# Kernel optimization log

Hardware: AMD Instinct MI355X
Metric: run time of the kernel (lower is better)

Reference implementation:

```python
import jax, jax.numpy as jnp
import numpy as np

B, T, D = 4, 2048, 1024
H = 16
DH = D // H

def setup_inputs() -> dict:
    key = jax.random.key(0)
    k1, k2, k3 = jax.random.split(key, 3)
    x = jax.random.normal(k1, (B, T, D), dtype=jnp.float32)
    causal_mask = jnp.tril(jnp.ones((T, T), dtype=bool))[None, None]  # (1,1,T,T)
    Wqkv = jax.random.normal(k2, (D, 3 * D), dtype=jnp.float32) * (1.0 / np.sqrt(D))
    Wout = jax.random.normal(k3, (D, D), dtype=jnp.float32) * (1.0 / np.sqrt(D))
    return {"x": x, "causal_mask": causal_mask, "Wqkv": Wqkv, "Wout": Wout}

def reference(x, causal_mask, Wqkv, Wout):
    Bb, Tt, C = x.shape
    scale = jnp.sqrt(jnp.asarray(DH, dtype=x.dtype))
    qkv = x @ Wqkv                                   # (B,T,3D)
    qkv = qkv.reshape(Bb, Tt, 3, H, DH)
    qkv = jnp.transpose(qkv, (2, 0, 3, 1, 4))        # (3,B,H,T,DH)
    q, k, v = qkv[0], qkv[1], qkv[2]
    attn = jnp.einsum('bhqd,bhkd->bhqk', q, k) / scale
    attn = jnp.where(causal_mask, attn, jnp.asarray(-jnp.inf, dtype=attn.dtype))
    attn = jax.nn.softmax(attn, axis=-1)             # dropout p=0 -> identity
    out = jnp.einsum('bhqk,bhkd->bhqd', attn, v)     # (B,H,T,DH)
    out = jnp.transpose(out, (0, 2, 1, 3)).reshape(Bb, Tt, C)
    return out @ Wout
```

## Files before the change

kernel.cpp:

```cpp
#include <hip/hip_runtime.h>
#include <hip/hip_bf16.h>
#include <math.h>


#define Bb 4
#define Tt 2048
#define Dd 1024
#define Hh 16
#define DH 64
#define Mrows (Bb*Tt)
#define NEGBIG (-1.0e30f)
#define KB64 (Dd/64)
#define CHUNKS 1024
#define TILEU16 8192

typedef unsigned short u16;
typedef __attribute__((ext_vector_type(8))) short bf16x8;
typedef __attribute__((ext_vector_type(4))) float f32x4;
typedef __attribute__((ext_vector_type(4))) unsigned int u32x4;

__device__ __forceinline__ u16 f2bf(float f) {
    union { float f; unsigned int i; } v; v.f = f;
    unsigned int x = v.i;
    return (u16)((x + 0x7fffu + ((x >> 16) & 1u)) >> 16);
}

__device__ __forceinline__ unsigned int cvt_pk_bf16(float lo, float hi) {
    unsigned int r;
    asm("v_cvt_pk_bf16_f32 %0, %1, %2" : "=v"(r) : "v"(lo), "v"(hi));
    return r;
}

__device__ __forceinline__ void perm32swap(unsigned& x, unsigned& y) {
    asm("v_permlane32_swap_b32 %0, %1" : "+v"(x), "+v"(y));
}
__device__ __forceinline__ void perm16swap(unsigned& x, unsigned& y) {
    asm("v_permlane16_swap_b32 %0, %1" : "+v"(x), "+v"(y));
}

__device__ __forceinline__ float exp2_(float x) {
#if __has_builtin(__builtin_amdgcn_exp2f)
    return __builtin_amdgcn_exp2f(x);
#else
    return __expf(x * 0.69314718056f);
#endif
}

typedef __attribute__((address_space(1))) const void glob_cv;
typedef __attribute__((address_space(3))) void lds_v;
__device__ __forceinline__ void gl2lds16(const void* g, void* l) {
    __builtin_amdgcn_global_load_lds((glob_cv*)g, (lds_v*)l, 16, 0, 0);
}

__device__ __forceinline__ void conv_w_body(const float* __restrict__ W,
                                            u16* __restrict__ Wt, int N,
                                            int nb, int kb, int tid,
                                            u16 (*t)[68]) {
    const int k0 = kb * 64, n0 = nb * 128;
    const int k = tid >> 2, ng = tid & 3;
    const float* s = W + (size_t)(k0 + k) * N + n0 + ng * 32;
    #pragma unroll
    for (int i = 0; i < 8; ++i) {
        float4 f = *(const float4*)(s + i * 4);
        const int n = ng * 32 + i * 4;
        t[n + 0][k] = f2bf(f.x); t[n + 1][k] = f2bf(f.y);
        t[n + 2][k] = f2bf(f.z); t[n + 3][k] = f2bf(f.w);
    }
    __syncthreads();
    u16* base = Wt + (size_t)(nb * KB64 + kb) * TILEU16;
    #pragma unroll
    for (int it = 0; it < 4; ++it) {
        const int c = it * 256 + tid;
        const int row = c & 127, kq = c >> 7;
        union { u16 u[8]; uint4 v; } o;
        #pragma unroll
        for (int j = 0; j < 8; ++j) o.u[j] = t[row][kq * 8 + j];
        *(uint4*)(base + (size_t)c * 8) = o.v;
    }
}

__global__ __launch_bounds__(256) void convert_all(const float* __restrict__ x,
                                                   const float* __restrict__ Wqkv,
                                                   const float* __restrict__ Wout,
                                                   u16* __restrict__ xT,
                                                   u16* __restrict__ WqkvT,
                                                   u16* __restrict__ WoutT) {
    __shared__ u16 t[128][68];
    const int bid = blockIdx.x, tid = threadIdx.x;
    if (bid < 1024) {
        const int mb = bid >> 4, kb = bid & 15;
        const int row = tid & 127, half = tid >> 7;
        const float* s = x + (size_t)(mb * 128 + row) * Dd + kb * 64 + half * 32;
        u16* base = xT + (size_t)bid * TILEU16;
        #pragma unroll
        for (int cq = 0; cq < 4; ++cq) {
            const int kq = half * 4 + cq;
            float4 f0 = *(const float4*)(s + cq * 8);
            float4 f1 = *(const float4*)(s + cq * 8 + 4);
            uint4 o;
            o.x = cvt_pk_bf16(f0.x, f0.y); o.y = cvt_pk_bf16(f0.z, f0.w);
            o.z = cvt_pk_bf16(f1.x, f1.y); o.w = cvt_pk_bf16(f1.z, f1.w);
            *(uint4*)(base + (size_t)(kq * 128 + row) * 8) = o;
        }
    } else if (bid < 1408) {
        const int r = bid - 1024;
        conv_w_body(Wqkv, WqkvT, 3 * Dd, r % 24, r / 24, tid, t);
    } else {
        const int r = bid - 1408;
        conv_w_body(Wout, WoutT, Dd, r % 8, r / 8, tid, t);
    }
}

template <int MODE>
__global__ __launch_bounds__(256) void gemm_mfma(const u16* __restrict__ At,
                                                 const u16* __restrict__ Bt,
                                                 u16* __restrict__ Qo,
                                                 u16* __restrict__ KT,
                                                 u16* __restrict__ VtT,
                                                 float* __restrict__ Out) {
    __shared__ u16 As[8 * 128 * 8];
    __shared__ u16 Bs[8 * 128 * 8];
    const int tid  = threadIdx.x;
    const int lane = tid & 63, w = tid >> 6;
    const int ml   = lane & 15, q = lane >> 4;
    const int wm   = w >> 1, wn = w & 1;

    const int nbx = gridDim.x;
    const int nwg = nbx * gridDim.y;
    int id = blockIdx.y * nbx + blockIdx.x;
    id = (id & 7) * (nwg >> 3) + (id >> 3);
    const int bxs = id % nbx, bys = id / nbx;

    const int m0 = bys * 128;
    const u16* Abase = At + (size_t)bys * KB64 * TILEU16;
    const u16* Bbase = Bt + (size_t)bxs * KB64 * TILEU16;

    f32x4 acc[4][4];
    #pragma unroll
    for (int i = 0; i < 4; ++i)
        #pragma unroll
        for (int j = 0; j < 4; ++j) acc[i][j] = (f32x4){0.f, 0.f, 0.f, 0.f};

    for (int kb = 0; kb < KB64; ++kb) {
        __syncthreads();
        const u16* Ak = Abase + (size_t)kb * TILEU16;
        const u16* Bk = Bbase + (size_t)kb * TILEU16;
        #pragma unroll
        for (int it = 0; it < 4; ++it) {
            const int c = it * 256 + tid;
            gl2lds16(Ak + (size_t)c * 8, (char*)As + c * 16);
            gl2lds16(Bk + (size_t)c * 8, (char*)Bs + c * 16);
        }
        __syncthreads();

        #pragma unroll
        for (int ks = 0; ks < 2; ++ks) {
            const int kq = ks * 4 + q;
            bf16x8 af[4], bfr[4];
            #pragma unroll
            for (int i = 0; i < 4; ++i)
                af[i] = *(const bf16x8*)((const char*)As +
                        ((kq * 128) + wm * 64 + i * 16 + ml) * 16);
            #pragma unroll
            for (int j = 0; j < 4; ++j)
                bfr[j] = *(const bf16x8*)((const char*)Bs +
                        ((kq * 128) + wn * 64 + j * 16 + ml) * 16);
            #pragma unroll
            for (int i = 0; i < 4; ++i)
                #pragma unroll
                for (int j = 0; j < 4; ++j)
                    acc[i][j] = __builtin_amdgcn_mfma_f32_16x16x32_bf16(
                            bfr[j], af[i], acc[i][j], 0, 0, 0);
        }
    }

    if (MODE == 0) {
        const int s  = (bxs * 128) >> 10;
        const int h0 = ((bxs * 128) & 1023) >> 6;
        #pragma unroll
        for (int i = 0; i < 4; ++i) {
            const int m  = m0 + wm * 64 + i * 16 + ml;
            const int bb = m >> 11, t = m & 2047;
            const int bhn = bb * Hh + h0 + wn;
            #pragma unroll
            for (int j = 0; j < 4; ++j) {
                const int dh = j * 16 + q * 4;
                if (s == 2) {
                    u16* vb = VtT + (size_t)(bhn * 16 + (t >> 7)) * TILEU16;
                    #pragma unroll
                    for (int r = 0; r < 4; ++r)
                        vb[(size_t)(((t >> 3) & 15) * 64 + dh + r) * 8 + (t & 7)]
                            = f2bf(acc[i][j][r]);
                } else if (s == 1) {
                    uint2 pk;
                    pk.x = cvt_pk_bf16(acc[i][j][0], acc[i][j][1]);
                    pk.y = cvt_pk_bf16(acc[i][j][2], acc[i][j][3]);
                    *(uint2*)(KT + (size_t)(bhn * 16 + (t >> 7)) * TILEU16 +
                              (size_t)((j * 2 + (q >> 1)) * 128 + (t & 127)) * 8 +
                              (q & 1) * 4) = pk;
                } else {
                    const float sc = 0.125f * 1.44269504089f;
                    uint2 pk;
                    pk.x = cvt_pk_bf16(acc[i][j][0] * sc, acc[i][j][1] * sc);
                    pk.y = cvt_pk_bf16(acc[i][j][2] * sc, acc[i][j][3] * sc);
                    *(uint2*)(Qo + ((size_t)bhn * Tt + t) * DH + dh) = pk;
                }
            }
        }
    } else {
        #pragma unroll
        for (int i = 0; i < 4; ++i) {
            const int m = m0 + wm * 64 + i * 16 + ml;
            #pragma unroll
            for (int j = 0; j < 4; ++j) {
                const int n = bxs * 128 + wn * 64 + j * 16 + q * 4;
                float4 st = {acc[i][j][0], acc[i][j][1], acc[i][j][2], acc[i][j][3]};
                *(float4*)(Out + (size_t)m * Dd + n) = st;
            }
        }
    }
}

__device__ __forceinline__ void softmax_pack(f32x4 (&st)[8], float& m_i, float& l_i,
                                             f32x4 (&accO)[4], unsigned (&d)[8],
                                             unsigned (&e)[8], int q, int qrow,
                                             bool diag) {
    if (diag) {
        #pragma unroll
        for (int kt = 0; kt < 8; ++kt)
            #pragma unroll
            for (int r = 0; r < 4; ++r)
                if (kt * 16 + q * 4 + r > qrow) st[kt][r] = NEGBIG;
    }
    float mx = NEGBIG;
    #pragma unroll
    for (int kt = 0; kt < 8; ++kt) {
        float a0 = fmaxf(st[kt][0], st[kt][1]);
        float a1 = fmaxf(st[kt][2], st[kt][3]);
        mx = fmaxf(fmaxf(mx, a0), a1);
    }
    mx = fmaxf(mx, __shfl_xor(mx, 16, 64));
    mx = fmaxf(mx, __shfl_xor(mx, 32, 64));

    float nm = m_i;
    if (__any(mx > m_i + 8.f)) {
        nm = fmaxf(m_i, mx);
        const float alpha = exp2_(m_i - nm);
        m_i = nm;
        l_i *= alpha;
        #pragma unroll
        for (int dt = 0; dt < 4; ++dt)
            #pragma unroll
            for (int r = 0; r < 4; ++r) accO[dt][r] *= alpha;
    }

    float rs = 0.f;
    #pragma unroll
    for (int kt = 0; kt < 8; ++kt) {
        const float p0 = exp2_(st[kt][0] - nm);
        const float p1 = exp2_(st[kt][1] - nm);
        const float p2 = exp2_(st[kt][2] - nm);
        const float p3 = exp2_(st[kt][3] - nm);
        rs += (p0 + p1) + (p2 + p3);
        d[kt] = cvt_pk_bf16(p0, p1);
        e[kt] = cvt_pk_bf16(p2, p3);
    }
    rs += __shfl_xor(rs, 16, 64);
    rs += __shfl_xor(rs, 32, 64);
    l_i += rs;
}

__device__ __forceinline__ bf16x8 build_bp(const unsigned (&d)[8],
                                           const unsigned (&e)[8], int s) {
    unsigned w0 = d[2 * s], w2 = d[2 * s + 1];
    perm32swap(w0, w2); perm16swap(w0, w2);
    unsigned w1 = e[2 * s], w3 = e[2 * s + 1];
    perm32swap(w1, w3); perm16swap(w1, w3);
    union { u32x4 u; bf16x8 b; } cv;
    cv.u = (u32x4){w0, w1, w2, w3};
    return cv.b;
}

__global__ __launch_bounds__(256, 3) void attn_mfma(const u16* __restrict__ Q,
                                                    const u16* __restrict__ KT,
                                                    const u16* __restrict__ VtT,
                                                    u16* __restrict__ AOT) {
    __shared__ u16 Ks[8 * 128 * 8];
    __shared__ u16 Vs[2][16 * 64 * 8];

    const int tid  = threadIdx.x;
    const int lane = tid & 63, w = tid >> 6;
    const int nl   = lane & 15, q = lane >> 4;

    int id = blockIdx.y * 8 + blockIdx.x;
    id = (id & 7) * 64 + (id >> 3);
    const int bxp = id & 7, bh = id >> 3;
    const int b = bh >> 4, h = bh & 15;
    const size_t kbase = (size_t)bh * Tt * DH;

    for (int phase = 0; phase < 2; ++phase) {
        const int qt = phase ? (15 - bxp) : bxp;
        const int q0 = qt * 128;
        const int nj = qt + 1;

        bf16x8 qf[2][2];
        #pragma unroll
        for (int qb = 0; qb < 2; ++qb)
            #pragma unroll
            for (int s = 0; s < 2; ++s)
                qf[qb][s] = *(const bf16x8*)(Q + kbase +
                        (size_t)(q0 + w * 32 + qb * 16 + nl) * DH + (s * 4 + q) * 8);

        float m_i[2] = {NEGBIG, NEGBIG};
        float l_i[2] = {0.f, 0.f};
        f32x4 accO[2][4];
        #pragma unroll
        for (int qb = 0; qb < 2; ++qb)
            #pragma unroll
            for (int dt = 0; dt < 4; ++dt) accO[qb][dt] = (f32x4){0.f, 0.f, 0.f, 0.f};

        __syncthreads();
        {
            const u16* Kb = KT  + (size_t)(bh * 16) * TILEU16;
            const u16* Vb = VtT + (size_t)(bh * 16) * TILEU16;
            #pragma unroll
            for (int it = 0; it < 4; ++it) {
                const int c = it * 256 + tid;
                gl2lds16(Kb + (size_t)c * 8, (char*)Ks + c * 16);
                gl2lds16(Vb + (size_t)c * 8, (char*)Vs[0] + c * 16);
            }
        }

        for (int jt = 0; jt < nj; ++jt) {
            const int buf = jt & 1;
            __syncthreads();

            f32x4 st0[8], st1[8];
            #pragma unroll
            for (int kt = 0; kt < 8; ++kt) {
                st0[kt] = (f32x4){0.f, 0.f, 0.f, 0.f};
                st1[kt] = (f32x4){0.f, 0.f, 0.f, 0.f};
            }
            __builtin_amdgcn_s_setprio(1);
            #pragma unroll
            for (int s = 0; s < 2; ++s) {
                #pragma unroll
                for (int kt = 0; kt < 8; ++kt) {
                    bf16x8 ak = *(const bf16x8*)((const char*)Ks +
                            ((s * 4 + q) * 128 + kt * 16 + nl) * 16);
                    st0[kt] = __builtin_amdgcn_mfma_f32_16x16x32_bf16(
                            ak, qf[0][s], st0[kt], 0, 0, 0);
                    st1[kt] = __builtin_amdgcn_mfma_f32_16x16x32_bf16(
                            ak, qf[1][s], st1[kt], 0, 0, 0);
                }
            }
            __builtin_amdgcn_s_setprio(0);

            __syncthreads();

            if (jt + 1 < nj) {
                const u16* Kb = KT  + (size_t)(bh * 16 + jt + 1) * TILEU16;
                const u16* Vb = VtT + (size_t)(bh * 16 + jt + 1) * TILEU16;
                #pragma unroll
                for (int it = 0; it < 4; ++it) {
                    const int c = it * 256 + tid;
                    gl2lds16(Kb + (size_t)c * 8, (char*)Ks + c * 16);
                    gl2lds16(Vb + (size_t)c * 8, (char*)Vs[buf ^ 1] + c * 16);
                }
            }

            const bool diag = (jt == nj - 1);
            unsigned d0[8], e0[8], d1[8], e1[8];
            softmax_pack(st0, m_i[0], l_i[0], accO[0], d0, e0, q, w * 32 + nl, diag);
            softmax_pack(st1, m_i[1], l_i[1], accO[1], d1, e1, q, w * 32 + 16 + nl, diag);

            __builtin_amdgcn_s_setprio(1);
            #pragma unroll
            for (int s = 0; s < 4; ++s) {
                bf16x8 bp0 = build_bp(d0, e0, s);
                bf16x8 bp1 = build_bp(d1, e1, s);
                #pragma unroll
                for (int dt = 0; dt < 4; ++dt) {
                    bf16x8 av = *(const bf16x8*)((const char*)Vs[buf] +
                            ((s * 4 + q) * 64 + dt * 16 + nl) * 16);
                    accO[0][dt] = __builtin_amdgcn_mfma_f32_16x16x32_bf16(
                            av, bp0, accO[0][dt], 0, 0, 0);
                    accO[1][dt] = __builtin_amdgcn_mfma_f32_16x16x32_bf16(
                            av, bp1, accO[1][dt], 0, 0, 0);
                }
            }
            __builtin_amdgcn_s_setprio(0);
        }

        #pragma unroll
        for (int qb = 0; qb < 2; ++qb) {
            const float inv = 1.0f / l_i[qb];
            const int t = q0 + w * 32 + qb * 16 + nl;
            const int m = b * Tt + t;
            u16* ab = AOT + (size_t)((m >> 7) * KB64 + h) * TILEU16;
            #pragma unroll
            for (int dt = 0; dt < 4; ++dt) {
                uint2 pk;
                pk.x = cvt_pk_bf16(accO[qb][dt][0] * inv, accO[qb][dt][1] * inv);
                pk.y = cvt_pk_bf16(accO[qb][dt][2] * inv, accO[qb][dt][3] * inv);
                *(uint2*)(ab + (size_t)((dt * 2 + (q >> 1)) * 128 + (m & 127)) * 8 +
                          (q & 1) * 4) = pk;
            }
        }
    }
}

extern "C" void kernel_launch(void* const* d_in, const int* in_sizes, int n_in,
                              void* d_out, int out_size, void* d_ws, size_t ws_size,
                              hipStream_t stream) {
    const float* x_raw    = (const float*)d_in[0];
    const float* Wqkv_raw = (const float*)d_in[2];
    const float* Wout_raw = (const float*)d_in[3];
    float* out = (float*)d_out;

    const size_t SZ = (size_t)Bb * Hh * Tt * DH;
    u16* ws = (u16*)d_ws;
    u16* Qw     = ws;
    u16* KT     = ws + SZ;
    u16* VtT    = ws + 2 * SZ;
    u16* AOT    = ws + 3 * SZ;
    u16* WqkvT  = ws + 4 * SZ;
    u16* WoutT  = WqkvT + (size_t)3 * Dd * Dd;
    u16* xT     = (u16*)d_out;

    convert_all<<<dim3(1536), 256, 0, stream>>>(x_raw, Wqkv_raw, Wout_raw,
                                                xT, WqkvT, WoutT);
    gemm_mfma<0><<<dim3(3 * Dd / 128, Mrows / 128), 256, 0, stream>>>(xT, WqkvT, Qw, KT, VtT, nullptr);
    attn_mfma  <<<dim3(Tt / 256, Bb * Hh), 256, 0, stream>>>(Qw, KT, VtT, AOT);
    gemm_mfma<1><<<dim3(Dd / 128, Mrows / 128), 256, 0, stream>>>(AOT, WoutT, nullptr, nullptr, nullptr, out);
}
```

Measured before the change: 269.8 us.

## Enlarge GEMM tile to 256x128 with 512 threads and triple-buffered async LDS pipeline

Both projection GEMMs now use 512-thread blocks that compute 256x128 output tiles, so each B tile loaded into shared memory is reused by twice as many rows. The K loop becomes a three-slot ring of global-to-LDS copies prefetched two steps ahead. It waits on vmcnt counters with a single barrier per step instead of two syncthreads, and splits the next stage's loads around the MFMA batches, which run at raised priority. The aim is to hide global load latency and cut barrier stalls. The cost is more LDS (about 96KB), higher register pressure under launch_bounds(512,2), and half as many workgroups.

Result: faster. 262.0 us (-2.9%).

```diff
diff --git a/kernel.cpp b/kernel.cpp
--- a/kernel.cpp
+++ b/kernel.cpp
@@ -112,18 +112,21 @@
 }
 
 template <int MODE>
-__global__ __launch_bounds__(256) void gemm_mfma(const u16* __restrict__ At,
-                                                 const u16* __restrict__ Bt,
-                                                 u16* __restrict__ Qo,
-                                                 u16* __restrict__ KT,
-                                                 u16* __restrict__ VtT,
-                                                 float* __restrict__ Out) {
-    __shared__ u16 As[8 * 128 * 8];
-    __shared__ u16 Bs[8 * 128 * 8];
+__global__ __launch_bounds__(512, 2) void gemm_mfma(const u16* __restrict__ At,
+                                                    const u16* __restrict__ Bt,
+                                                    u16* __restrict__ Qo,
+                                                    u16* __restrict__ KT,
+                                                    u16* __restrict__ VtT,
+                                                    float* __restrict__ Out) {
+    __shared__ u16 As[3][2][8 * 128 * 8];
+    __shared__ u16 Bs[3][8 * 128 * 8];
+
     const int tid  = threadIdx.x;
     const int lane = tid & 63, w = tid >> 6;
     const int ml   = lane & 15, q = lane >> 4;
     const int wm   = w >> 1, wn = w & 1;
+    const int mh   = wm >> 1;
+    const int mrow = (wm & 1) * 64;
 
     const int nbx = gridDim.x;
     const int nwg = nbx * gridDim.y;
@@ -131,9 +134,9 @@
     id = (id & 7) * (nwg >> 3) + (id >> 3);
     const int bxs = id % nbx, bys = id / nbx;
 
-    const int m0 = bys * 128;
-    const u16* Abase = At + (size_t)bys * KB64 * TILEU16;
-    const u16* Bbase = Bt + (size_t)bxs * KB64 * TILEU16;
+    const u16* A0 = At + (size_t)(2 * bys)     * KB64 * TILEU16;
+    const u16* A1 = At + (size_t)(2 * bys + 1) * KB64 * TILEU16;
+    const u16* B0 = Bt + (size_t)bxs           * KB64 * TILEU16;
 
     f32x4 acc[4][4];
     #pragma unroll
@@ -141,45 +144,79 @@
         #pragma unroll
         for (int j = 0; j < 4; ++j) acc[i][j] = (f32x4){0.f, 0.f, 0.f, 0.f};
 
-    for (int kb = 0; kb < KB64; ++kb) {
-        __syncthreads();
-        const u16* Ak = Abase + (size_t)kb * TILEU16;
-        const u16* Bk = Bbase + (size_t)kb * TILEU16;
-        #pragma unroll
-        for (int it = 0; it < 4; ++it) {
-            const int c = it * 256 + tid;
-            gl2lds16(Ak + (size_t)c * 8, (char*)As + c * 16);
-            gl2lds16(Bk + (size_t)c * 8, (char*)Bs + c * 16);
-        }
-        __syncthreads();
-
+    #define STAGE_A(k_, sl_, it_) do {                                        \
+        const int c_ = (it_) * 512 + tid;                                     \
+        const int h_ = c_ >> 10, cc_ = c_ & 1023;                             \
+        gl2lds16((h_ ? A1 : A0) + (size_t)(k_) * TILEU16 + (size_t)cc_ * 8,   \
+                 (char*)As[sl_][h_] + (size_t)cc_ * 16);                      \
+    } while (0)
+    #define STAGE_B(k_, sl_, it_) do {                                        \
+        const int c_ = (it_) * 512 + tid;                                     \
+        gl2lds16(B0 + (size_t)(k_) * TILEU16 + (size_t)c_ * 8,                \
+                 (char*)Bs[sl_] + (size_t)c_ * 16);                           \
+    } while (0)
+
+    STAGE_A(0, 0, 0); STAGE_A(0, 0, 1); STAGE_A(0, 0, 2); STAGE_A(0, 0, 3);
+    STAGE_B(0, 0, 0); STAGE_B(0, 0, 1);
+    STAGE_A(1, 1, 0); STAGE_A(1, 1, 1); STAGE_A(1, 1, 2); STAGE_A(1, 1, 3);
+    STAGE_B(1, 1, 0); STAGE_B(1, 1, 1);
+
+    for (int k = 0; k < KB64; ++k) {
+        const int sl = k % 3;
+        if (k == KB64 - 1) asm volatile("s_waitcnt vmcnt(0)" ::: "memory");
+        else               asm volatile("s_waitcnt vmcnt(6)" ::: "memory");
+        __builtin_amdgcn_s_barrier();
+
+        const int k2 = k + 2, s2 = k2 % 3;
+        if (k2 < KB64) { STAGE_A(k2, s2, 0); STAGE_A(k2, s2, 1); STAGE_B(k2, s2, 0); }
+
+        bf16x8 bfr[4][2], af[4][2];
         #pragma unroll
         for (int ks = 0; ks < 2; ++ks) {
             const int kq = ks * 4 + q;
-            bf16x8 af[4], bfr[4];
+            #pragma unroll
+            for (int j = 0; j < 4; ++j)
+                bfr[j][ks] = *(const bf16x8*)((const char*)Bs[sl] +
+                        ((kq * 128) + wn * 64 + j * 16 + ml) * 16);
             #pragma unroll
             for (int i = 0; i < 4; ++i)
-                af[i] = *(const bf16x8*)((const char*)As +
-                        ((kq * 128) + wm * 64 + i * 16 + ml) * 16);
+                af[i][ks] = *(const bf16x8*)((const char*)As[sl][mh] +
+                        ((kq * 128) + mrow + i * 16 + ml) * 16);
+        }
+
+        __builtin_amdgcn_s_setprio(1);
+        #pragma unroll
+        for (int i = 0; i < 2; ++i)
             #pragma unroll
             for (int j = 0; j < 4; ++j)
-                bfr[j] = *(const bf16x8*)((const char*)Bs +
-                        ((kq * 128) + wn * 64 + j * 16 + ml) * 16);
-            #pragma unroll
-            for (int i = 0; i < 4; ++i)
                 #pragma unroll
-                for (int j = 0; j < 4; ++j)
+                for (int ks = 0; ks < 2; ++ks)
                     acc[i][j] = __builtin_amdgcn_mfma_f32_16x16x32_bf16(
-                            bfr[j], af[i], acc[i][j], 0, 0, 0);
-        }
-    }
+                            bfr[j][ks], af[i][ks], acc[i][j], 0, 0, 0);
+        __builtin_amdgcn_s_setprio(0);
+
+        if (k2 < KB64) { STAGE_A(k2, s2, 2); STAGE_A(k2, s2, 3); STAGE_B(k2, s2, 1); }
+
+        __builtin_amdgcn_s_setprio(1);
+        #pragma unroll
+        for (int i = 2; i < 4; ++i)
+            #pragma unroll
+            for (int j = 0; j < 4; ++j)
+                #pragma unroll
+                for (int ks = 0; ks < 2; ++ks)
+                    acc[i][j] = __builtin_amdgcn_mfma_f32_16x16x32_bf16(
+                            bfr[j][ks], af[i][ks], acc[i][j], 0, 0, 0);
+        __builtin_amdgcn_s_setprio(0);
+    }
+    #undef STAGE_A
+    #undef STAGE_B
 
     if (MODE == 0) {
         const int s  = (bxs * 128) >> 10;
         const int h0 = ((bxs * 128) & 1023) >> 6;
         #pragma unroll
         for (int i = 0; i < 4; ++i) {
-            const int m  = m0 + wm * 64 + i * 16 + ml;
+            const int m  = bys * 256 + wm * 64 + i * 16 + ml;
             const int bb = m >> 11, t = m & 2047;
             const int bhn = bb * Hh + h0 + wn;
             #pragma unroll
@@ -210,7 +247,7 @@
     } else {
         #pragma unroll
         for (int i = 0; i < 4; ++i) {
-            const int m = m0 + wm * 64 + i * 16 + ml;
+            const int m = bys * 256 + wm * 64 + i * 16 + ml;
             #pragma unroll
             for (int j = 0; j < 4; ++j) {
                 const int n = bxs * 128 + wn * 64 + j * 16 + q * 4;
@@ -430,7 +467,7 @@
 
     convert_all<<<dim3(1536), 256, 0, stream>>>(x_raw, Wqkv_raw, Wout_raw,
                                                 xT, WqkvT, WoutT);
-    gemm_mfma<0><<<dim3(3 * Dd / 128, Mrows / 128), 256, 0, stream>>>(xT, WqkvT, Qw, KT, VtT, nullptr);
+    gemm_mfma<0><<<dim3(3 * Dd / 128, Mrows / 256), 512, 0, stream>>>(xT, WqkvT, Qw, KT, VtT, nullptr);
     attn_mfma  <<<dim3(Tt / 256, Bb * Hh), 256, 0, stream>>>(Qw, KT, VtT, AOT);
-    gemm_mfma<1><<<dim3(Dd / 128, Mrows / 128), 256, 0, stream>>>(AOT, WoutT, nullptr, nullptr, nullptr, out);
-}
+    gemm_mfma<1><<<dim3(Dd / 128, Mrows / 256), 512, 0, stream>>>(AOT, WoutT, nullptr, nullptr, nullptr, out);
+}
```
